# Optimization experiments

Hardware: AMD Instinct MI355X
Metric: run time of the kernel (lower is better)

The kernel has to match this reference:

```python
import jax, jax.numpy as jnp
import numpy as np

B, T, D_IN = 2048, 26, 512
H = 512          # hidden_size
E = 256          # num_char_embeddings
C = 97           # num_class
S = 32           # num_steps = batch_max_length + 1


def setup_inputs() -> dict:
    key = jax.random.key(0)
    ks = jax.random.split(key, 16)
    sc = lambda n: 1.0 / np.sqrt(n)
    inp = {
        "batch_H": jax.random.normal(ks[0], (B, T, D_IN), jnp.float32),
        "text": jax.random.randint(ks[1], (B, S), 0, C),
        # attention cell params
        "W_i2h": jax.random.normal(ks[2], (H, D_IN), jnp.float32) * sc(D_IN),
        "W_h2h": jax.random.normal(ks[3], (H, H), jnp.float32) * sc(H),
        "b_h2h": jax.random.normal(ks[4], (H,), jnp.float32) * sc(H),
        "w_score": jax.random.normal(ks[5], (1, H), jnp.float32) * sc(H),
        # LSTMCell params (gate order: i, f, g, o)
        "W_ih": jax.random.normal(ks[6], (4 * H, D_IN + E), jnp.float32) * sc(D_IN + E),
        "W_hh": jax.random.normal(ks[7], (4 * H, H), jnp.float32) * sc(H),
        "b_ih": jax.random.normal(ks[8], (4 * H,), jnp.float32) * sc(H),
        "b_hh": jax.random.normal(ks[9], (4 * H,), jnp.float32) * sc(H),
        # generator + char embedding
        "W_gen": jax.random.normal(ks[10], (C, H), jnp.float32) * sc(H),
        "b_gen": jax.random.normal(ks[11], (C,), jnp.float32) * sc(H),
        "emb_table": jax.random.normal(ks[12], (C, E), jnp.float32),
    }
    return inp


def _decode(batch_H, text, W_i2h, W_h2h, b_h2h, w_score,
            W_ih, W_hh, b_ih, b_hh, emb_table):
    # i2h(batch_H) is constant across steps -> hoist out of the loop
    Hp = jnp.einsum('btd,hd->bth', batch_H, W_i2h)          # [B,T,H]
    char_embs = emb_table[text]                              # [B,S,E]
    h0 = jnp.zeros((batch_H.shape[0], H), batch_H.dtype)
    c0 = jnp.zeros_like(h0)

    def step(carry, ce):
        h, c = carry
        ph = h @ W_h2h.T + b_h2h                             # [B,H]
        e = jnp.tanh(Hp + ph[:, None, :]) @ w_score[0]       # [B,T]
        alpha = jax.nn.softmax(e, axis=1)                    # [B,T]
        context = jnp.einsum('bt,btd->bd', alpha, batch_H)   # [B,D_IN]
        x = jnp.concatenate([context, ce], axis=1)           # [B,D_IN+E]
        gates = x @ W_ih.T + b_ih + h @ W_hh.T + b_hh        # [B,4H]
        i, f, g, o = jnp.split(gates, 4, axis=1)
        c_new = jax.nn.sigmoid(f) * c + jax.nn.sigmoid(i) * jnp.tanh(g)
        h_new = jax.nn.sigmoid(o) * jnp.tanh(c_new)
        return (h_new, c_new), h_new

    _, hs = jax.lax.scan(step, (h0, c0), jnp.swapaxes(char_embs, 0, 1))
    return jnp.swapaxes(hs, 0, 1)                            # [B,S,H]


def reference(batch_H, text, W_i2h, W_h2h, b_h2h, w_score,
              W_ih, W_hh, b_ih, b_hh, W_gen, b_gen, emb_table):
    output_hiddens = _decode(batch_H, text, W_i2h, W_h2h, b_h2h, w_score,
                             W_ih, W_hh, b_ih, b_hh, emb_table)
    probs = output_hiddens @ W_gen.T + b_gen                 # [B,S,C]
    return probs
```

## Files before the change

### kernel.cpp

```cpp
#include <hip/hip_runtime.h>

#define BB 2048
#define TT 26
#define DIN 512
#define HH 512
#define EE 256
#define CC 97
#define SS 32
#define G4 2048
#define XK2 1024

typedef unsigned short u16;
typedef __bf16 bf16x8 __attribute__((ext_vector_type(8)));
typedef float f32x4 __attribute__((ext_vector_type(4)));

__device__ __forceinline__ float bf2f(u16 u) {
    return __uint_as_float(((unsigned int)u) << 16);
}
__device__ __forceinline__ u16 f2bf(float f) {
    unsigned int u = __float_as_uint(f);
    u = u + 0x7FFFu + ((u >> 16) & 1u);
    return (u16)(u >> 16);
}
__device__ __forceinline__ float th_f(float x) {
    return 1.0f - 2.0f * __builtin_amdgcn_rcpf(__expf(2.0f * x) + 1.0f);
}
__device__ __forceinline__ float sig_f(float x) {
    return __builtin_amdgcn_rcpf(1.0f + __expf(-x));
}

__device__ __forceinline__ void async16(const u16* g, u16* l) {
    __builtin_amdgcn_global_load_lds(
        (const __attribute__((address_space(1))) unsigned int*)(g),
        (__attribute__((address_space(3))) unsigned int*)(l), 16, 0, 0);
}

__global__ __launch_bounds__(256) void gemm128(
    const u16* __restrict__ A, int lda,
    const u16* __restrict__ W,
    u16* __restrict__ Cout, int ldc, int K)
{
    __shared__ __align__(16) u16 As[128 * 32];
    __shared__ __align__(16) u16 Ws[128 * 32];

    const int tid  = threadIdx.x;
    const int lane = tid & 63;
    const int wave = tid >> 6;
    const int m0 = blockIdx.y * 128;
    const int n0 = blockIdx.x * 128;

    const int srow = tid >> 2;
    const int scol = (tid & 3) * 8;
    const u16* Arow0 = A + (size_t)(m0 + srow) * lda + scol;
    const u16* Arow1 = A + (size_t)(m0 + 64 + srow) * lda + scol;
    const u16* Wrow0 = W + (size_t)(n0 + srow) * K + scol;
    const u16* Wrow1 = W + (size_t)(n0 + 64 + srow) * K + scol;
    u16* dstA0 = As + wave * 512;
    u16* dstA1 = As + 2048 + wave * 512;
    u16* dstW0 = Ws + wave * 512;
    u16* dstW1 = Ws + 2048 + wave * 512;

    const int wm = (wave >> 1) * 64;
    const int wn = (wave & 1) * 64;
    const int fr = lane & 15;
    const int fq = lane >> 4;

    f32x4 acc[4][4];
    #pragma unroll
    for (int i = 0; i < 4; i++)
        #pragma unroll
        for (int j = 0; j < 4; j++)
            #pragma unroll
            for (int r = 0; r < 4; r++) acc[i][j][r] = 0.0f;

    for (int k0 = 0; k0 < K; k0 += 32) {
        async16(Arow0 + k0, dstA0);
        async16(Arow1 + k0, dstA1);
        async16(Wrow0 + k0, dstW0);
        async16(Wrow1 + k0, dstW1);
        __syncthreads();
        bf16x8 af[4], bw[4];
        #pragma unroll
        for (int i = 0; i < 4; i++)
            af[i] = *(const bf16x8*)&As[(wm + i * 16 + fr) * 32 + fq * 8];
        #pragma unroll
        for (int j = 0; j < 4; j++)
            bw[j] = *(const bf16x8*)&Ws[(wn + j * 16 + fr) * 32 + fq * 8];
        #pragma unroll
        for (int i = 0; i < 4; i++)
            #pragma unroll
            for (int j = 0; j < 4; j++)
                acc[i][j] = __builtin_amdgcn_mfma_f32_16x16x32_bf16(
                    af[i], bw[j], acc[i][j], 0, 0, 0);
        __syncthreads();
    }

    #pragma unroll
    for (int j = 0; j < 4; j++) {
        int col = n0 + wn + j * 16 + fr;
        #pragma unroll
        for (int i = 0; i < 4; i++) {
            int row = m0 + wm + i * 16 + fq * 4;
            #pragma unroll
            for (int r = 0; r < 4; r++)
                Cout[(size_t)(row + r) * ldc + col] = f2bf(acc[i][j][r]);
        }
    }
}

__global__ __launch_bounds__(256) void gen128(
    const u16* __restrict__ A,
    const u16* __restrict__ Wg,
    const float* __restrict__ bgen,
    float* __restrict__ out)
{
    __shared__ __align__(16) u16 As[128 * 32];
    __shared__ __align__(16) u16 Ws[128 * 32];

    const int tid  = threadIdx.x;
    const int lane = tid & 63;
    const int wave = tid >> 6;
    const int m0 = blockIdx.y * 128;

    const int srow = tid >> 2;
    const int scol = (tid & 3) * 8;
    const u16* Arow0 = A + (size_t)(m0 + srow) * HH + scol;
    const u16* Arow1 = A + (size_t)(m0 + 64 + srow) * HH + scol;
    const u16* Wrow0 = Wg + (size_t)srow * HH + scol;
    const u16* Wrow1 = Wg + (size_t)(64 + srow) * HH + scol;
    u16* dstA0 = As + wave * 512;
    u16* dstA1 = As + 2048 + wave * 512;
    u16* dstW0 = Ws + wave * 512;
    u16* dstW1 = Ws + 2048 + wave * 512;

    const int wm = (wave >> 1) * 64;
    const int wn = (wave & 1) * 64;
    const int fr = lane & 15;
    const int fq = lane >> 4;

    f32x4 acc[4][4];
    #pragma unroll
    for (int i = 0; i < 4; i++)
        #pragma unroll
        for (int j = 0; j < 4; j++)
            #pragma unroll
            for (int r = 0; r < 4; r++) acc[i][j][r] = 0.0f;

    for (int k0 = 0; k0 < HH; k0 += 32) {
        async16(Arow0 + k0, dstA0);
        async16(Arow1 + k0, dstA1);
        async16(Wrow0 + k0, dstW0);
        async16(Wrow1 + k0, dstW1);
        __syncthreads();
        bf16x8 af[4], bw[4];
        #pragma unroll
        for (int i = 0; i < 4; i++)
            af[i] = *(const bf16x8*)&As[(wm + i * 16 + fr) * 32 + fq * 8];
        #pragma unroll
        for (int j = 0; j < 4; j++)
            bw[j] = *(const bf16x8*)&Ws[(wn + j * 16 + fr) * 32 + fq * 8];
        #pragma unroll
        for (int i = 0; i < 4; i++)
            #pragma unroll
            for (int j = 0; j < 4; j++)
                acc[i][j] = __builtin_amdgcn_mfma_f32_16x16x32_bf16(
                    af[i], bw[j], acc[i][j], 0, 0, 0);
        __syncthreads();
    }

    #pragma unroll
    for (int j = 0; j < 4; j++) {
        int col = wn + j * 16 + fr;
        if (col < CC) {
            float bv = bgen[col];
            #pragma unroll
            for (int i = 0; i < 4; i++) {
                int row = m0 + wm + i * 16 + fq * 4;
                #pragma unroll
                for (int r = 0; r < 4; r++) {
                    int m = row + r;
                    int s = m >> 11, b = m & (BB - 1);
                    out[(size_t)b * (SS * CC) + s * CC + col] = acc[i][j][r] + bv;
                }
            }
        }
    }
}

__global__ __launch_bounds__(256) void gates_lstm(
    const u16* __restrict__ ctx,
    const u16* __restrict__ hprev,
    const u16* __restrict__ Wc,
    const float* __restrict__ bcat,
    const float* __restrict__ P,
    const int* __restrict__ text,
    float* __restrict__ c,
    u16* __restrict__ hnext,
    int s)
{
    __shared__ __align__(16) u16 As[64 * 32];
    __shared__ __align__(16) u16 Ws[128 * 32];
    __shared__ float gsm[64 * 68];
    __shared__ int text_sm[64];

    const int tid  = threadIdx.x;
    const int lane = tid & 63;
    const int wave = tid >> 6;

    int b   = blockIdx.y * gridDim.x + blockIdx.x;
    int xcd = b & 7, loc = b >> 3;
    int by = (xcd & 3) * 8 + (loc & 7);
    int bx = (xcd >> 2) * 8 + (loc >> 3);
    const int m0 = by * 64;
    const int n0 = bx * 128;

    if (tid < 64) text_sm[tid] = text[(m0 + tid) * SS + s];

    const int srow = tid >> 2;
    const int scol = (tid & 3) * 8;
    const u16* Actx  = ctx   + (size_t)(m0 + srow) * 512 + scol;
    const u16* Ahid  = hprev + (size_t)(m0 + srow) * 512 + scol;
    const u16* Wrow0 = Wc + (size_t)(n0 + srow) * XK2 + scol;
    const u16* Wrow1 = Wc + (size_t)(n0 + 64 + srow) * XK2 + scol;
    u16* dstA  = As + wave * 512;
    u16* dstW0 = Ws + wave * 512;
    u16* dstW1 = Ws + 2048 + wave * 512;

    const int wm = (wave & 1) * 32;
    const int wn = (wave >> 1) * 64;
    const int fr = lane & 15;
    const int fq = lane >> 4;

    f32x4 acc[2][4];
    #pragma unroll
    for (int i = 0; i < 2; i++)
        #pragma unroll
        for (int j = 0; j < 4; j++)
            #pragma unroll
            for (int r = 0; r < 4; r++) acc[i][j][r] = 0.0f;

    #pragma unroll
    for (int k0 = 0; k0 < XK2; k0 += 32) {
        const u16* asrc = (k0 < 512) ? (Actx + k0) : (Ahid + (k0 - 512));
        async16(asrc, dstA);
        async16(Wrow0 + k0, dstW0);
        async16(Wrow1 + k0, dstW1);
        __syncthreads();
        bf16x8 af[2], bw[4];
        #pragma unroll
        for (int i = 0; i < 2; i++)
            af[i] = *(const bf16x8*)&As[(wm + i * 16 + fr) * 32 + fq * 8];
        #pragma unroll
        for (int j = 0; j < 4; j++)
            bw[j] = *(const bf16x8*)&Ws[(wn + j * 16 + fr) * 32 + fq * 8];
        #pragma unroll
        for (int i = 0; i < 2; i++)
            #pragma unroll
            for (int j = 0; j < 4; j++)
                acc[i][j] = __builtin_amdgcn_mfma_f32_16x16x32_bf16(
                    af[i], bw[j], acc[i][j], 0, 0, 0);
        __syncthreads();
    }

    #pragma unroll
    for (int p = 0; p < 2; p++) {
        if ((wave >> 1) == p) {
            #pragma unroll
            for (int j = 0; j < 4; j++) {
                int cl = j * 16 + fr;
                #pragma unroll
                for (int i = 0; i < 2; i++) {
                    int rl = wm + i * 16 + fq * 4;
                    #pragma unroll
                    for (int r = 0; r < 4; r++)
                        gsm[(rl + r) * 68 + cl] = acc[i][j][r];
                }
            }
        }
        __syncthreads();
        #pragma unroll
        for (int rr = 0; rr < 4; rr++) {
            int idx = rr * 256 + tid;
            int u = idx & 15, row = idx >> 4;
            int base = row * 68 + 4 * u;
            int hg = (n0 >> 2) + p * 16 + u;
            int c0 = 4 * hg;
            int ch = text_sm[row];
            float4 bc = *(const float4*)(bcat + c0);
            float4 pv = *(const float4*)(P + (size_t)ch * G4 + c0);
            float ig = sig_f(gsm[base]     + bc.x + pv.x);
            float fg = sig_f(gsm[base + 1] + bc.y + pv.y);
            float gg = th_f (gsm[base + 2] + bc.z + pv.z);
            float og = sig_f(gsm[base + 3] + bc.w + pv.w);
            size_t ci = (size_t)(m0 + row) * HH + hg;
            float cn = fg * c[ci] + ig * gg;
            c[ci] = cn;
            hnext[(size_t)(m0 + row) * HH + hg] = f2bf(og * th_f(cn));
        }
        __syncthreads();
    }
}

__global__ __launch_bounds__(256) void gemm64(
    const u16* __restrict__ A, int lda,
    const u16* __restrict__ W, int ldw,
    const float* __restrict__ bias,
    float* __restrict__ Cout, int ldc, int K, int use_bias)
{
    __shared__ __align__(16) u16 As[64][32];
    __shared__ __align__(16) u16 Ws[64][32];

    const int tid  = threadIdx.x;
    const int lane = tid & 63;
    const int wave = tid >> 6;
    const int m0 = blockIdx.y * 64;
    const int n0 = blockIdx.x * 64;
    const int ar = tid >> 2;
    const int ac = (tid & 3) * 8;
    const int wm = (wave >> 1) * 32;
    const int wn = (wave & 1) * 32;
    const int fr = lane & 15;
    const int fq = lane >> 4;

    f32x4 acc[2][2];
    #pragma unroll
    for (int i = 0; i < 2; i++)
        #pragma unroll
        for (int j = 0; j < 2; j++)
            #pragma unroll
            for (int r = 0; r < 4; r++) acc[i][j][r] = 0.0f;

    const u16* Arow = A + (size_t)(m0 + ar) * lda;
    const u16* Wrow = W + (size_t)(n0 + ar) * ldw;

    for (int k0 = 0; k0 < K; k0 += 32) {
        *(uint4*)&As[ar][ac] = *(const uint4*)(Arow + k0 + ac);
        *(uint4*)&Ws[ar][ac] = *(const uint4*)(Wrow + k0 + ac);
        __syncthreads();
        bf16x8 af[2], bw[2];
        #pragma unroll
        for (int mm = 0; mm < 2; mm++)
            af[mm] = *(const bf16x8*)&As[wm + mm * 16 + fr][fq * 8];
        #pragma unroll
        for (int nn = 0; nn < 2; nn++)
            bw[nn] = *(const bf16x8*)&Ws[wn + nn * 16 + fr][fq * 8];
        #pragma unroll
        for (int mm = 0; mm < 2; mm++)
            #pragma unroll
            for (int nn = 0; nn < 2; nn++)
                acc[mm][nn] = __builtin_amdgcn_mfma_f32_16x16x32_bf16(
                    af[mm], bw[nn], acc[mm][nn], 0, 0, 0);
        __syncthreads();
    }

    #pragma unroll
    for (int nn = 0; nn < 2; nn++) {
        int col = n0 + wn + nn * 16 + fr;
        float bv = use_bias ? bias[col] : 0.0f;
        #pragma unroll
        for (int mm = 0; mm < 2; mm++) {
            int row = m0 + wm + mm * 16 + fq * 4;
            #pragma unroll
            for (int r = 0; r < 4; r++)
                Cout[(size_t)(row + r) * ldc + col] = acc[mm][nn][r] + bv;
        }
    }
}

__global__ __launch_bounds__(256) void attn_step(
    const u16* __restrict__ Hp, const float* __restrict__ ph,
    const float* __restrict__ wscore, const u16* __restrict__ bH16,
    u16* __restrict__ ctx)
{
    const int b = blockIdx.x;
    const int tid = threadIdx.x, lane = tid & 63, wave = tid >> 6;
    __shared__ float e_sm[32];
    __shared__ float alpha_sm[32];

    const int h8 = lane * 8;
    float ph_r[8], ws_r[8];
    {
        float4 p0 = *(const float4*)(ph + (size_t)b * HH + h8);
        float4 p1 = *(const float4*)(ph + (size_t)b * HH + h8 + 4);
        ph_r[0]=p0.x; ph_r[1]=p0.y; ph_r[2]=p0.z; ph_r[3]=p0.w;
        ph_r[4]=p1.x; ph_r[5]=p1.y; ph_r[6]=p1.z; ph_r[7]=p1.w;
        float4 w0 = *(const float4*)(wscore + h8);
        float4 w1 = *(const float4*)(wscore + h8 + 4);
        ws_r[0]=w0.x; ws_r[1]=w0.y; ws_r[2]=w0.z; ws_r[3]=w0.w;
        ws_r[4]=w1.x; ws_r[5]=w1.y; ws_r[6]=w1.z; ws_r[7]=w1.w;
    }

    for (int t = wave; t < TT; t += 4) {
        uint4 hv = *(const uint4*)(Hp + ((size_t)b * TT + t) * HH + h8);
        const u16* hu = (const u16*)&hv;
        float sum = 0.0f;
        #pragma unroll
        for (int j = 0; j < 8; j++)
            sum += th_f(bf2f(hu[j]) + ph_r[j]) * ws_r[j];
        #pragma unroll
        for (int off = 32; off > 0; off >>= 1) sum += __shfl_down(sum, off);
        if (lane == 0) e_sm[t] = sum;
    }
    __syncthreads();

    if (wave == 0) {
        float ev = (lane < TT) ? e_sm[lane] : -3.0e38f;
        float mx = ev;
        #pragma unroll
        for (int off = 32; off > 0; off >>= 1)
            mx = fmaxf(mx, __shfl_xor(mx, off));
        float p = (lane < TT) ? __expf(ev - mx) : 0.0f;
        float ssum = p;
        #pragma unroll
        for (int off = 32; off > 0; off >>= 1) ssum += __shfl_xor(ssum, off);
        if (lane < TT) alpha_sm[lane] = p / ssum;
    }
    __syncthreads();

    {
        int d0 = tid * 2;
        float c0 = 0.0f, c1 = 0.0f;
        const u16* bb = bH16 + (size_t)b * TT * DIN + d0;
        #pragma unroll
        for (int t = 0; t < TT; t++) {
            unsigned int v = *(const unsigned int*)(bb + (size_t)t * DIN);
            float a = alpha_sm[t];
            c0 += a * bf2f((u16)(v & 0xffffu));
            c1 += a * bf2f((u16)(v >> 16));
        }
        unsigned int o = (unsigned int)f2bf(c0) | ((unsigned int)f2bf(c1) << 16);
        *(unsigned int*)(ctx + (size_t)b * 512 + d0) = o;
    }
}

__global__ __launch_bounds__(256) void cast_f32_bf16(
    const float* __restrict__ src, u16* __restrict__ dst, int n)
{
    int i = (blockIdx.x * 256 + threadIdx.x) * 4;
    if (i < n) {
        float4 v = *(const float4*)(src + i);
        ushort4 o;
        o.x = f2bf(v.x); o.y = f2bf(v.y); o.z = f2bf(v.z); o.w = f2bf(v.w);
        *(ushort4*)(dst + i) = o;
    }
}

__global__ __launch_bounds__(256) void prep_all(
    const float* __restrict__ W_ih, const float* __restrict__ W_hh,
    const float* __restrict__ b_ih, const float* __restrict__ b_hh,
    const float* __restrict__ b_h2h, const float* __restrict__ emb,
    const float* __restrict__ W_i2h, const float* __restrict__ W_h2h,
    const float* __restrict__ W_gen,
    u16* __restrict__ Wcat, u16* __restrict__ Wce16, u16* __restrict__ emb16,
    u16* __restrict__ Wgen16, u16* __restrict__ Wi2h16, u16* __restrict__ Wh2h16,
    float* __restrict__ bcat, float* __restrict__ cst, u16* __restrict__ hid0,
    float* __restrict__ ph)
{
    int i = blockIdx.x * 256 + threadIdx.x;

    {
        int np = i >> 10, k = i & (XK2 - 1);
        int h = np >> 2, g = np & 3;
        int n = g * HH + h;
        float v = (k < 512) ? W_ih[(size_t)n * (DIN + EE) + k]
                            : W_hh[(size_t)n * HH + (k - 512)];
        Wcat[(size_t)i] = f2bf(v);
    }
    if (i < G4 * EE) {
        int np = i >> 8, e = i & (EE - 1);
        int h = np >> 2, g = np & 3;
        int n = g * HH + h;
        Wce16[i] = f2bf(W_ih[(size_t)n * (DIN + EE) + DIN + e]);
    }
    if (i < 128 * EE) {
        int ch = i >> 8, e = i & (EE - 1);
        emb16[i] = (ch < CC) ? f2bf(emb[(size_t)ch * EE + e]) : (u16)0;
    }
    if (i < 128 * HH) {
        int n = i >> 9, k = i & (HH - 1);
        Wgen16[i] = (n < CC) ? f2bf(W_gen[(size_t)n * HH + k]) : (u16)0;
    }
    if (i < HH * DIN) Wi2h16[i] = f2bf(W_i2h[i]);
    if (i < HH * HH)  Wh2h16[i] = f2bf(W_h2h[i]);
    if (i < G4) {
        int h = i >> 2, g = i & 3;
        int n = g * HH + h;
        bcat[i] = b_ih[n] + b_hh[n];
    }
    if (i < BB * HH) {
        cst[i] = 0.0f;
        hid0[i] = 0;
        ph[i] = b_h2h[i & (HH - 1)];
    }
}

#define BH16_OFF  ((size_t)0)
#define HP_OFF    ((size_t)54525952)
#define HID_OFF   ((size_t)109051904)
#define CTX_OFF   ((size_t)178257920)
#define WCAT_OFF  ((size_t)180355072)
#define WCE_OFF   ((size_t)184549376)
#define EMB16_OFF ((size_t)185597952)
#define WGEN_OFF  ((size_t)185663488)
#define WI2H_OFF  ((size_t)185794560)
#define WH2H_OFF  ((size_t)186318848)
#define BCAT_OFF  ((size_t)186843136)
#define P_OFF     ((size_t)186851328)
#define PH_OFF    ((size_t)187899904)
#define CST_OFF   ((size_t)192094208)

extern "C" void kernel_launch(void* const* d_in, const int* in_sizes, int n_in,
                              void* d_out, int out_size, void* d_ws, size_t ws_size,
                              hipStream_t stream)
{
    const float* batch_H = (const float*)d_in[0];
    const int*   text    = (const int*)d_in[1];
    const float* W_i2h   = (const float*)d_in[2];
    const float* W_h2h   = (const float*)d_in[3];
    const float* b_h2h   = (const float*)d_in[4];
    const float* w_score = (const float*)d_in[5];
    const float* W_ih    = (const float*)d_in[6];
    const float* W_hh    = (const float*)d_in[7];
    const float* b_ih    = (const float*)d_in[8];
    const float* b_hh    = (const float*)d_in[9];
    const float* W_gen   = (const float*)d_in[10];
    const float* b_gen   = (const float*)d_in[11];
    const float* emb     = (const float*)d_in[12];

    char* ws = (char*)d_ws;
    u16*   bH16   = (u16*)(ws + BH16_OFF);
    u16*   Hp     = (u16*)(ws + HP_OFF);
    u16*   hid    = (u16*)(ws + HID_OFF);
    u16*   ctx    = (u16*)(ws + CTX_OFF);
    u16*   Wcat   = (u16*)(ws + WCAT_OFF);
    u16*   Wce16  = (u16*)(ws + WCE_OFF);
    u16*   emb16  = (u16*)(ws + EMB16_OFF);
    u16*   Wgen16 = (u16*)(ws + WGEN_OFF);
    u16*   Wi2h16 = (u16*)(ws + WI2H_OFF);
    u16*   Wh2h16 = (u16*)(ws + WH2H_OFF);
    float* bcat   = (float*)(ws + BCAT_OFF);
    float* P      = (float*)(ws + P_OFF);
    float* ph     = (float*)(ws + PH_OFF);
    float* cst    = (float*)(ws + CST_OFF);
    float* out    = (float*)d_out;

    cast_f32_bf16<<<dim3((BB * TT * DIN / 4 + 255) / 256), 256, 0, stream>>>(
        batch_H, bH16, BB * TT * DIN);
    prep_all<<<dim3((G4 * XK2) / 256), 256, 0, stream>>>(
        W_ih, W_hh, b_ih, b_hh, b_h2h, emb, W_i2h, W_h2h, W_gen,
        Wcat, Wce16, emb16, Wgen16, Wi2h16, Wh2h16, bcat, cst, hid, ph);
    gemm64<<<dim3(G4 / 64, 128 / 64), 256, 0, stream>>>(
        emb16, EE, Wce16, EE, nullptr, P, G4, EE, 0);

    gemm128<<<dim3(HH / 128, (BB * TT) / 128), 256, 0, stream>>>(
        bH16, DIN, Wi2h16, Hp, HH, DIN);

    for (int s = 0; s < SS; s++) {
        u16* hprev = hid + (size_t)s * BB * HH;
        u16* hnext = hid + (size_t)(s + 1) * BB * HH;

        attn_step<<<dim3(BB), 256, 0, stream>>>(Hp, ph, w_score, bH16, ctx);

        gates_lstm<<<dim3(G4 / 128, BB / 64), 256, 0, stream>>>(
            ctx, hprev, Wcat, bcat, P, text, cst, hnext, s);

        gemm64<<<dim3(HH / 64, BB / 64), 256, 0, stream>>>(
            hnext, HH, Wh2h16, HH, b_h2h, ph, HH, HH, 1);
    }

    gen128<<<dim3(1, (SS * BB) / 128), 256, 0, stream>>>(
        hid + (size_t)BB * HH, Wgen16, b_gen, out);
}
```

Before: 1.805 ms.

## Fuse recurrent decode loop into one persistent kernel with grid barriers

Replaces the 96 per-step kernel launches (attention, gates/LSTM, h2h GEMM) with one persistent kernel of 1024 blocks that loops over all 32 steps, separating phases with a software grid barrier built on atomics. The LSTM cell state is kept in registers across steps instead of in global memory, and the h2h projection is recomputed at the start of each step. This removes launch overhead and inter-kernel gaps but depends on all blocks being co-resident (checked through an occupancy query with fallback to the old path) and adds spin-barrier cost three times per step with smaller tiles.

```diff
diff --git a/kernel.cpp b/kernel.cpp
--- a/kernel.cpp
+++ b/kernel.cpp
@@ -9,6 +9,7 @@
 #define SS 32
 #define G4 2048
 #define XK2 1024
+#define NBLK 1024
 
 typedef unsigned short u16;
 typedef __bf16 bf16x8 __attribute__((ext_vector_type(8)));
@@ -33,6 +34,252 @@
     __builtin_amdgcn_global_load_lds(
         (const __attribute__((address_space(1))) unsigned int*)(g),
         (__attribute__((address_space(3))) unsigned int*)(l), 16, 0, 0);
+}
+
+__device__ __forceinline__ void gridbar(unsigned int* cnt, unsigned int* gen) {
+    __syncthreads();
+    if (threadIdx.x == 0) {
+        unsigned int g = __hip_atomic_load(gen, __ATOMIC_RELAXED, __HIP_MEMORY_SCOPE_AGENT);
+        unsigned int v = __hip_atomic_fetch_add(cnt, 1u, __ATOMIC_ACQ_REL, __HIP_MEMORY_SCOPE_AGENT);
+        if (v == (unsigned int)(NBLK - 1)) {
+            __hip_atomic_store(cnt, 0u, __ATOMIC_RELAXED, __HIP_MEMORY_SCOPE_AGENT);
+            __hip_atomic_store(gen, g + 1u, __ATOMIC_RELEASE, __HIP_MEMORY_SCOPE_AGENT);
+        } else {
+            while (__hip_atomic_load(gen, __ATOMIC_ACQUIRE, __HIP_MEMORY_SCOPE_AGENT) == g)
+                __builtin_amdgcn_s_sleep(2);
+        }
+    }
+    __syncthreads();
+    __threadfence();
+}
+
+__global__ __launch_bounds__(256, 4) void persist(
+    u16* hid,
+    const u16* __restrict__ Wh,
+    const float* __restrict__ bh2h,
+    const u16* __restrict__ Hp,
+    const u16* __restrict__ bH16,
+    const float* __restrict__ wscore,
+    u16* ctx,
+    float* phg,
+    const u16* __restrict__ Wc,
+    const float* __restrict__ bcat,
+    const float* __restrict__ P,
+    const int* __restrict__ text,
+    unsigned int* bar)
+{
+    __shared__ __align__(16) char smem[32768];
+    __shared__ float e_sm[2][32];
+    __shared__ float alpha_sm[2][32];
+    __shared__ int text_sm[64];
+
+    u16* smA = (u16*)smem;
+    u16* smB = (u16*)(smem + 16384);
+    float* gsm = (float*)smem;
+
+    const int tid  = threadIdx.x;
+    const int lane = tid & 63;
+    const int wave = tid >> 6;
+    const int bid  = blockIdx.x;
+    const int fr = lane & 15;
+    const int fq = lane >> 4;
+
+    unsigned int* bcnt = bar;
+    unsigned int* bgen = bar + 32;
+
+    const int p1_m0 = (bid >> 4) * 32;
+    const int p1_n0 = (bid & 15) * 32;
+    const int p3_m0 = (bid >> 5) * 64;
+    const int p3_nt = bid & 31;
+    const int p3_n0 = p3_nt * 64;
+
+    float c_reg[4] = {0.0f, 0.0f, 0.0f, 0.0f};
+
+    for (int s = 0; s < SS; s++) {
+        const u16* hid_s = hid + (size_t)s * BB * HH;
+        u16* hid_n = hid + (size_t)(s + 1) * BB * HH;
+
+        {
+            f32x4 acc1;
+            #pragma unroll
+            for (int r = 0; r < 4; r++) acc1[r] = 0.0f;
+            const int wm = (wave >> 1) * 16, wn = (wave & 1) * 16;
+            #pragma unroll
+            for (int cchunk = 0; cchunk < 2; cchunk++) {
+                int kc = cchunk * 256;
+                #pragma unroll
+                for (int j = 0; j < 4; j++) {
+                    int row = j * 8 + wave * 2 + (lane >> 5);
+                    int col = ((lane & 31) ^ (row & 7)) * 8;
+                    async16(hid_s + (size_t)(p1_m0 + row) * 512 + kc + col,
+                            smA + j * 2048 + wave * 512);
+                    async16(Wh + (size_t)(p1_n0 + row) * 512 + kc + col,
+                            smB + j * 2048 + wave * 512);
+                }
+                __syncthreads();
+                #pragma unroll
+                for (int kk = 0; kk < 8; kk++) {
+                    int ra = wm + fr, rb = wn + fr;
+                    bf16x8 af = *(const bf16x8*)(smem + ra * 512 +
+                                                 (((kk * 4 + fq) ^ (ra & 7)) * 16));
+                    bf16x8 bw = *(const bf16x8*)(smem + 16384 + rb * 512 +
+                                                 (((kk * 4 + fq) ^ (rb & 7)) * 16));
+                    acc1 = __builtin_amdgcn_mfma_f32_16x16x32_bf16(af, bw, acc1, 0, 0, 0);
+                }
+                __syncthreads();
+            }
+            int coln = p1_n0 + wn + fr;
+            float bv = bh2h[coln];
+            #pragma unroll
+            for (int r = 0; r < 4; r++)
+                phg[(size_t)(p1_m0 + wm + fq * 4 + r) * 512 + coln] = acc1[r] + bv;
+        }
+        gridbar(bcnt, bgen);
+
+        {
+            const int rloc = wave >> 1;
+            const int wv = wave & 1;
+            const int b = bid * 2 + rloc;
+            const int h8 = lane * 8;
+            float ph_r[8], ws_r[8];
+            {
+                float4 p0 = *(const float4*)(phg + (size_t)b * HH + h8);
+                float4 p1 = *(const float4*)(phg + (size_t)b * HH + h8 + 4);
+                ph_r[0]=p0.x; ph_r[1]=p0.y; ph_r[2]=p0.z; ph_r[3]=p0.w;
+                ph_r[4]=p1.x; ph_r[5]=p1.y; ph_r[6]=p1.z; ph_r[7]=p1.w;
+                float4 w0 = *(const float4*)(wscore + h8);
+                float4 w1 = *(const float4*)(wscore + h8 + 4);
+                ws_r[0]=w0.x; ws_r[1]=w0.y; ws_r[2]=w0.z; ws_r[3]=w0.w;
+                ws_r[4]=w1.x; ws_r[5]=w1.y; ws_r[6]=w1.z; ws_r[7]=w1.w;
+            }
+            const u16* hpb = Hp + (size_t)b * TT * 512 + h8;
+            for (int t = wv; t < TT; t += 2) {
+                uint4 hv = *(const uint4*)(hpb + (size_t)t * 512);
+                const u16* hu = (const u16*)&hv;
+                float sum = 0.0f;
+                #pragma unroll
+                for (int j = 0; j < 8; j++)
+                    sum += th_f(bf2f(hu[j]) + ph_r[j]) * ws_r[j];
+                #pragma unroll
+                for (int off = 32; off > 0; off >>= 1) sum += __shfl_down(sum, off);
+                if (lane == 0) e_sm[rloc][t] = sum;
+            }
+            __syncthreads();
+            if (wv == 0) {
+                float ev = (lane < TT) ? e_sm[rloc][lane] : -3.0e38f;
+                float mx = ev;
+                #pragma unroll
+                for (int off = 32; off > 0; off >>= 1)
+                    mx = fmaxf(mx, __shfl_xor(mx, off));
+                float p = (lane < TT) ? __expf(ev - mx) : 0.0f;
+                float ssum = p;
+                #pragma unroll
+                for (int off = 32; off > 0; off >>= 1) ssum += __shfl_xor(ssum, off);
+                if (lane < TT) alpha_sm[rloc][lane] = p / ssum;
+            }
+            __syncthreads();
+            {
+                int d0 = (wv * 64 + lane) * 4;
+                float ca0 = 0.f, ca1 = 0.f, ca2 = 0.f, ca3 = 0.f;
+                const u16* bb = bH16 + (size_t)b * TT * DIN + d0;
+                #pragma unroll
+                for (int t = 0; t < TT; t++) {
+                    uint2 v = *(const uint2*)(bb + (size_t)t * DIN);
+                    float a = alpha_sm[rloc][t];
+                    ca0 += a * bf2f((u16)(v.x & 0xffffu));
+                    ca1 += a * bf2f((u16)(v.x >> 16));
+                    ca2 += a * bf2f((u16)(v.y & 0xffffu));
+                    ca3 += a * bf2f((u16)(v.y >> 16));
+                }
+                uint2 o;
+                o.x = (unsigned int)f2bf(ca0) | ((unsigned int)f2bf(ca1) << 16);
+                o.y = (unsigned int)f2bf(ca2) | ((unsigned int)f2bf(ca3) << 16);
+                *(uint2*)(ctx + (size_t)b * 512 + d0) = o;
+            }
+        }
+        gridbar(bcnt, bgen);
+
+        {
+            if (tid < 64) text_sm[tid] = text[(p3_m0 + tid) * SS + s];
+            f32x4 acc[2][2];
+            #pragma unroll
+            for (int i = 0; i < 2; i++)
+                #pragma unroll
+                for (int j = 0; j < 2; j++)
+                    #pragma unroll
+                    for (int r = 0; r < 4; r++) acc[i][j][r] = 0.0f;
+            const int wm = (wave & 1) * 32, wn = (wave >> 1) * 32;
+
+            for (int chk = 0; chk < 8; chk++) {
+                int kc = chk * 128;
+                #pragma unroll
+                for (int j = 0; j < 4; j++) {
+                    int row = j * 16 + wave * 4 + (lane >> 4);
+                    int col = ((lane & 15) ^ (row & 7)) * 8;
+                    const u16* asrc = (kc < 512)
+                        ? (const u16*)(ctx + (size_t)(p3_m0 + row) * 512 + kc + col)
+                        : (hid_s + (size_t)(p3_m0 + row) * 512 + (kc - 512) + col);
+                    async16(asrc, smA + j * 2048 + wave * 512);
+                    async16(Wc + (size_t)(p3_n0 + row) * XK2 + kc + col,
+                            smB + j * 2048 + wave * 512);
+                }
+                __syncthreads();
+                #pragma unroll
+                for (int kk = 0; kk < 4; kk++) {
+                    bf16x8 af[2], bw[2];
+                    #pragma unroll
+                    for (int i = 0; i < 2; i++) {
+                        int ra = wm + i * 16 + fr;
+                        af[i] = *(const bf16x8*)(smem + ra * 256 +
+                                                 (((kk * 4 + fq) ^ (ra & 7)) * 16));
+                    }
+                    #pragma unroll
+                    for (int j = 0; j < 2; j++) {
+                        int rb = wn + j * 16 + fr;
+                        bw[j] = *(const bf16x8*)(smem + 16384 + rb * 256 +
+                                                 (((kk * 4 + fq) ^ (rb & 7)) * 16));
+                    }
+                    #pragma unroll
+                    for (int i = 0; i < 2; i++)
+                        #pragma unroll
+                        for (int j = 0; j < 2; j++)
+                            acc[i][j] = __builtin_amdgcn_mfma_f32_16x16x32_bf16(
+                                af[i], bw[j], acc[i][j], 0, 0, 0);
+                }
+                __syncthreads();
+            }
+            #pragma unroll
+            for (int i = 0; i < 2; i++)
+                #pragma unroll
+                for (int j = 0; j < 2; j++) {
+                    int rl = wm + i * 16 + fq * 4;
+                    int cl = wn + j * 16 + fr;
+                    #pragma unroll
+                    for (int r = 0; r < 4; r++)
+                        gsm[(rl + r) * 68 + cl] = acc[i][j][r];
+                }
+            __syncthreads();
+            #pragma unroll
+            for (int rr = 0; rr < 4; rr++) {
+                int idx = rr * 256 + tid;
+                int u = idx & 15, row = idx >> 4;
+                int hg = p3_nt * 16 + u;
+                int c0 = 4 * hg;
+                int chv = text_sm[row];
+                float4 bc = *(const float4*)(bcat + c0);
+                float4 pv = *(const float4*)(P + (size_t)chv * G4 + c0);
+                const float* gb = &gsm[row * 68 + 4 * u];
+                float ig = sig_f(gb[0] + bc.x + pv.x);
+                float fg = sig_f(gb[1] + bc.y + pv.y);
+                float gg = th_f (gb[2] + bc.z + pv.z);
+                float og = sig_f(gb[3] + bc.w + pv.w);
+                float cn = fg * c_reg[rr] + ig * gg;
+                c_reg[rr] = cn;
+                hid_n[(size_t)(p3_m0 + row) * HH + hg] = f2bf(og * th_f(cn));
+            }
+        }
+        gridbar(bcnt, bgen);
+    }
 }
 
 __global__ __launch_bounds__(256) void gemm128(
@@ -188,15 +435,10 @@
 }
 
 __global__ __launch_bounds__(256) void gates_lstm(
-    const u16* __restrict__ ctx,
-    const u16* __restrict__ hprev,
-    const u16* __restrict__ Wc,
-    const float* __restrict__ bcat,
-    const float* __restrict__ P,
-    const int* __restrict__ text,
-    float* __restrict__ c,
-    u16* __restrict__ hnext,
-    int s)
+    const u16* __restrict__ ctx, const u16* __restrict__ hprev,
+    const u16* __restrict__ Wc, const float* __restrict__ bcat,
+    const float* __restrict__ P, const int* __restrict__ text,
+    float* __restrict__ c, u16* __restrict__ hnext, int s)
 {
     __shared__ __align__(16) u16 As[64 * 32];
     __shared__ __align__(16) u16 Ws[128 * 32];
@@ -454,7 +696,7 @@
     u16* __restrict__ Wcat, u16* __restrict__ Wce16, u16* __restrict__ emb16,
     u16* __restrict__ Wgen16, u16* __restrict__ Wi2h16, u16* __restrict__ Wh2h16,
     float* __restrict__ bcat, float* __restrict__ cst, u16* __restrict__ hid0,
-    float* __restrict__ ph)
+    float* __restrict__ ph, unsigned int* __restrict__ bar)
 {
     int i = blockIdx.x * 256 + threadIdx.x;
 
@@ -492,6 +734,7 @@
         hid0[i] = 0;
         ph[i] = b_h2h[i & (HH - 1)];
     }
+    if (i < 64) bar[i] = 0u;
 }
 
 #define BH16_OFF  ((size_t)0)
@@ -508,6 +751,7 @@
 #define P_OFF     ((size_t)186851328)
 #define PH_OFF    ((size_t)187899904)
 #define CST_OFF   ((size_t)192094208)
+#define BAR_OFF   ((size_t)196288512)
 
 extern "C" void kernel_launch(void* const* d_in, const int* in_sizes, int n_in,
                               void* d_out, int out_size, void* d_ws, size_t ws_size,
@@ -542,30 +786,42 @@
     float* P      = (float*)(ws + P_OFF);
     float* ph     = (float*)(ws + PH_OFF);
     float* cst    = (float*)(ws + CST_OFF);
+    unsigned int* bar = (unsigned int*)(ws + BAR_OFF);
     float* out    = (float*)d_out;
 
     cast_f32_bf16<<<dim3((BB * TT * DIN / 4 + 255) / 256), 256, 0, stream>>>(
         batch_H, bH16, BB * TT * DIN);
     prep_all<<<dim3((G4 * XK2) / 256), 256, 0, stream>>>(
         W_ih, W_hh, b_ih, b_hh, b_h2h, emb, W_i2h, W_h2h, W_gen,
-        Wcat, Wce16, emb16, Wgen16, Wi2h16, Wh2h16, bcat, cst, hid, ph);
+        Wcat, Wce16, emb16, Wgen16, Wi2h16, Wh2h16, bcat, cst, hid, ph, bar);
     gemm64<<<dim3(G4 / 64, 128 / 64), 256, 0, stream>>>(
         emb16, EE, Wce16, EE, nullptr, P, G4, EE, 0);
 
     gemm128<<<dim3(HH / 128, (BB * TT) / 128), 256, 0, stream>>>(
         bH16, DIN, Wi2h16, Hp, HH, DIN);
 
-    for (int s = 0; s < SS; s++) {
-        u16* hprev = hid + (size_t)s * BB * HH;
-        u16* hnext = hid + (size_t)(s + 1) * BB * HH;
-
-        attn_step<<<dim3(BB), 256, 0, stream>>>(Hp, ph, w_score, bH16, ctx);
-
-        gates_lstm<<<dim3(G4 / 128, BB / 64), 256, 0, stream>>>(
-            ctx, hprev, Wcat, bcat, P, text, cst, hnext, s);
-
-        gemm64<<<dim3(HH / 64, BB / 64), 256, 0, stream>>>(
-            hnext, HH, Wh2h16, HH, b_h2h, ph, HH, HH, 1);
+    static int s_occ = -1;
+    if (s_occ < 0) {
+        int occ = 0;
+        if (hipOccupancyMaxActiveBlocksPerMultiprocessor(&occ, persist, 256, 0)
+            != hipSuccess) occ = 0;
+        s_occ = occ;
+    }
+
+    if (s_occ >= 4) {
+        persist<<<dim3(NBLK), 256, 0, stream>>>(
+            hid, Wh2h16, b_h2h, Hp, bH16, w_score, ctx, ph,
+            Wcat, bcat, P, text, bar);
+    } else {
+        for (int s = 0; s < SS; s++) {
+            u16* hprev = hid + (size_t)s * BB * HH;
+            u16* hnext = hid + (size_t)(s + 1) * BB * HH;
+            attn_step<<<dim3(BB), 256, 0, stream>>>(Hp, ph, w_score, bH16, ctx);
+            gates_lstm<<<dim3(G4 / 128, BB / 64), 256, 0, stream>>>(
+                ctx, hprev, Wcat, bcat, P, text, cst, hnext, s);
+            gemm64<<<dim3(HH / 64, BB / 64), 256, 0, stream>>>(
+                hnext, HH, Wh2h16, HH, b_h2h, ph, HH, HH, 1);
+        }
     }
 
     gen128<<<dim3(1, (SS * BB) / 128), 256, 0, stream>>>(
```

After: 1.804 ms. No clear change (-0.1%).

## Enlarge gates_lstm tile to 128x128 with double-buffered LDS and swizzle gemm128 blocks

Applied to the files above, without the earlier changes.

The per-step gates+LSTM kernel now computes a 128x128 tile per block with a 4x4 MFMA accumulator per wave. Its K loop double-buffers the async global-to-LDS loads so the next slice is prefetched while the current one is computed, and the LSTM epilogue runs in a single pass over a shared 128x132 buffer. The hoisted Hp GEMM also gets an XCD-aware block remap for better L2 locality. The larger tile halves the grid to 256 blocks and raises register and LDS use, which may lower occupancy.

```diff
diff --git a/kernel.cpp b/kernel.cpp
--- a/kernel.cpp
+++ b/kernel.cpp
@@ -46,8 +46,11 @@
     const int tid  = threadIdx.x;
     const int lane = tid & 63;
     const int wave = tid >> 6;
-    const int m0 = blockIdx.y * 128;
-    const int n0 = blockIdx.x * 128;
+
+    int b = blockIdx.y * 4 + blockIdx.x;
+    int swz = (b & 7) * 208 + (b >> 3);
+    const int m0 = (swz >> 2) * 128;
+    const int n0 = (swz & 3) * 128;
 
     const int srow = tid >> 2;
     const int scol = (tid & 3) * 8;
@@ -198,106 +201,112 @@
     u16* __restrict__ hnext,
     int s)
 {
-    __shared__ __align__(16) u16 As[64 * 32];
-    __shared__ __align__(16) u16 Ws[128 * 32];
-    __shared__ float gsm[64 * 68];
-    __shared__ int text_sm[64];
+    __shared__ __align__(16) char smem[128 * 132 * 4];
+    __shared__ int text_sm[128];
 
     const int tid  = threadIdx.x;
     const int lane = tid & 63;
     const int wave = tid >> 6;
 
-    int b   = blockIdx.y * gridDim.x + blockIdx.x;
+    int b   = blockIdx.y * 16 + blockIdx.x;
     int xcd = b & 7, loc = b >> 3;
-    int by = (xcd & 3) * 8 + (loc & 7);
-    int bx = (xcd >> 2) * 8 + (loc >> 3);
-    const int m0 = by * 64;
+    int by = (xcd & 3) * 4 + (loc & 3);
+    int bx = (xcd >> 2) * 8 + (loc >> 2);
+    const int m0 = by * 128;
     const int n0 = bx * 128;
 
-    if (tid < 64) text_sm[tid] = text[(m0 + tid) * SS + s];
+    if (tid < 128) text_sm[tid] = text[(m0 + tid) * SS + s];
 
     const int srow = tid >> 2;
     const int scol = (tid & 3) * 8;
-    const u16* Actx  = ctx   + (size_t)(m0 + srow) * 512 + scol;
-    const u16* Ahid  = hprev + (size_t)(m0 + srow) * 512 + scol;
+    const u16* Actx0 = ctx   + (size_t)(m0 + srow) * 512 + scol;
+    const u16* Actx1 = ctx   + (size_t)(m0 + 64 + srow) * 512 + scol;
+    const u16* Ahid0 = hprev + (size_t)(m0 + srow) * 512 + scol;
+    const u16* Ahid1 = hprev + (size_t)(m0 + 64 + srow) * 512 + scol;
     const u16* Wrow0 = Wc + (size_t)(n0 + srow) * XK2 + scol;
     const u16* Wrow1 = Wc + (size_t)(n0 + 64 + srow) * XK2 + scol;
-    u16* dstA  = As + wave * 512;
-    u16* dstW0 = Ws + wave * 512;
-    u16* dstW1 = Ws + 2048 + wave * 512;
-
-    const int wm = (wave & 1) * 32;
-    const int wn = (wave >> 1) * 64;
+
+    const int wm = (wave >> 1) * 64;
+    const int wn = (wave & 1) * 64;
     const int fr = lane & 15;
     const int fq = lane >> 4;
 
-    f32x4 acc[2][4];
-    #pragma unroll
-    for (int i = 0; i < 2; i++)
+    f32x4 acc[4][4];
+    #pragma unroll
+    for (int i = 0; i < 4; i++)
         #pragma unroll
         for (int j = 0; j < 4; j++)
             #pragma unroll
             for (int r = 0; r < 4; r++) acc[i][j][r] = 0.0f;
 
-    #pragma unroll
-    for (int k0 = 0; k0 < XK2; k0 += 32) {
-        const u16* asrc = (k0 < 512) ? (Actx + k0) : (Ahid + (k0 - 512));
-        async16(asrc, dstA);
-        async16(Wrow0 + k0, dstW0);
-        async16(Wrow1 + k0, dstW1);
-        __syncthreads();
-        bf16x8 af[2], bw[4];
-        #pragma unroll
-        for (int i = 0; i < 2; i++)
-            af[i] = *(const bf16x8*)&As[(wm + i * 16 + fr) * 32 + fq * 8];
+    #define STAGE_GATES(kk, bufsel)                                          \
+        {                                                                    \
+            int k0_ = (kk) * 32;                                             \
+            u16* As_ = (u16*)(smem + (bufsel) * 16384);                      \
+            u16* Ws_ = (u16*)(smem + (bufsel) * 16384 + 8192);               \
+            const u16* a0_ = (k0_ < 512) ? Actx0 + k0_ : Ahid0 + (k0_ - 512);\
+            const u16* a1_ = (k0_ < 512) ? Actx1 + k0_ : Ahid1 + (k0_ - 512);\
+            async16(a0_, As_ + wave * 512);                                  \
+            async16(a1_, As_ + 2048 + wave * 512);                           \
+            async16(Wrow0 + k0_, Ws_ + wave * 512);                          \
+            async16(Wrow1 + k0_, Ws_ + 2048 + wave * 512);                   \
+        }
+
+    STAGE_GATES(0, 0);
+    #pragma unroll 2
+    for (int it = 0; it < 32; it++) {
+        __syncthreads();
+        if (it + 1 < 32) STAGE_GATES(it + 1, (it + 1) & 1);
+        const u16* As_ = (const u16*)(smem + (it & 1) * 16384);
+        const u16* Ws_ = (const u16*)(smem + (it & 1) * 16384 + 8192);
+        bf16x8 af[4], bw[4];
+        #pragma unroll
+        for (int i = 0; i < 4; i++)
+            af[i] = *(const bf16x8*)&As_[(wm + i * 16 + fr) * 32 + fq * 8];
         #pragma unroll
         for (int j = 0; j < 4; j++)
-            bw[j] = *(const bf16x8*)&Ws[(wn + j * 16 + fr) * 32 + fq * 8];
-        #pragma unroll
-        for (int i = 0; i < 2; i++)
+            bw[j] = *(const bf16x8*)&Ws_[(wn + j * 16 + fr) * 32 + fq * 8];
+        #pragma unroll
+        for (int i = 0; i < 4; i++)
             #pragma unroll
             for (int j = 0; j < 4; j++)
                 acc[i][j] = __builtin_amdgcn_mfma_f32_16x16x32_bf16(
                     af[i], bw[j], acc[i][j], 0, 0, 0);
-        __syncthreads();
-    }
-
-    #pragma unroll
-    for (int p = 0; p < 2; p++) {
-        if ((wave >> 1) == p) {
-            #pragma unroll
-            for (int j = 0; j < 4; j++) {
-                int cl = j * 16 + fr;
-                #pragma unroll
-                for (int i = 0; i < 2; i++) {
-                    int rl = wm + i * 16 + fq * 4;
-                    #pragma unroll
-                    for (int r = 0; r < 4; r++)
-                        gsm[(rl + r) * 68 + cl] = acc[i][j][r];
-                }
-            }
+    }
+    __syncthreads();
+    #undef STAGE_GATES
+
+    float* gsm = (float*)smem;
+    #pragma unroll
+    for (int i = 0; i < 4; i++)
+        #pragma unroll
+        for (int j = 0; j < 4; j++) {
+            int rl = wm + i * 16 + fq * 4;
+            int cl = wn + j * 16 + fr;
+            #pragma unroll
+            for (int r = 0; r < 4; r++)
+                gsm[(rl + r) * 132 + cl] = acc[i][j][r];
         }
-        __syncthreads();
-        #pragma unroll
-        for (int rr = 0; rr < 4; rr++) {
-            int idx = rr * 256 + tid;
-            int u = idx & 15, row = idx >> 4;
-            int base = row * 68 + 4 * u;
-            int hg = (n0 >> 2) + p * 16 + u;
-            int c0 = 4 * hg;
-            int ch = text_sm[row];
-            float4 bc = *(const float4*)(bcat + c0);
-            float4 pv = *(const float4*)(P + (size_t)ch * G4 + c0);
-            float ig = sig_f(gsm[base]     + bc.x + pv.x);
-            float fg = sig_f(gsm[base + 1] + bc.y + pv.y);
-            float gg = th_f (gsm[base + 2] + bc.z + pv.z);
-            float og = sig_f(gsm[base + 3] + bc.w + pv.w);
-            size_t ci = (size_t)(m0 + row) * HH + hg;
-            float cn = fg * c[ci] + ig * gg;
-            c[ci] = cn;
-            hnext[(size_t)(m0 + row) * HH + hg] = f2bf(og * th_f(cn));
-        }
-        __syncthreads();
+    __syncthreads();
+
+    #pragma unroll
+    for (int rr = 0; rr < 16; rr++) {
+        int idx = rr * 256 + tid;
+        int u = idx & 31, row = idx >> 5;
+        int hg = bx * 32 + u;
+        int cb = 4 * hg;
+        int ch = text_sm[row];
+        float4 bc = *(const float4*)(bcat + cb);
+        float4 pv = *(const float4*)(P + (size_t)ch * G4 + cb);
+        const float* gb = &gsm[row * 132 + 4 * u];
+        float ig = sig_f(gb[0] + bc.x + pv.x);
+        float fg = sig_f(gb[1] + bc.y + pv.y);
+        float gg = th_f (gb[2] + bc.z + pv.z);
+        float og = sig_f(gb[3] + bc.w + pv.w);
+        size_t ci = (size_t)(m0 + row) * HH + hg;
+        float cn = fg * c[ci] + ig * gg;
+        c[ci] = cn;
+        hnext[ci] = f2bf(og * th_f(cn));
     }
 }
 
@@ -561,7 +570,7 @@
 
         attn_step<<<dim3(BB), 256, 0, stream>>>(Hp, ph, w_score, bH16, ctx);
 
-        gates_lstm<<<dim3(G4 / 128, BB / 64), 256, 0, stream>>>(
+        gates_lstm<<<dim3(16, 16), 256, 0, stream>>>(
             ctx, hprev, Wcat, bcat, P, text, cst, hnext, s);
 
         gemm64<<<dim3(HH / 64, BB / 64), 256, 0, stream>>>(
```

New measurement: 1.937 ms. 7.4% more time.
